# Performance work log

Measured on AMD Instinct MI355X. Metric: run time of the kernel, lower is better.

Reference implementation:

```python
import jax, jax.numpy as jnp
import numpy as np

N_SIN = 3  # fcn_n_sin

def _feats(x):
    # x: [B, Din] -> features [B, Din, 1 + 2*N_SIN]
    omega = (2.0 ** jnp.arange(N_SIN, dtype=x.dtype))  # [n_sin]
    ox = x[..., None] * omega  # [B, Din, n_sin]
    return jnp.concatenate([x[..., None], jnp.sin(ox), jnp.cos(ox)], axis=-1)

def setup_inputs() -> dict:
    key = jax.random.key(0)
    k1, k2, k3 = jax.random.split(key, 3)
    B, Din, Dout, H, F = 2048, 64, 64, 32, 1 + 2 * N_SIN
    x = jax.random.normal(k1, (B, Din), dtype=jnp.float32)
    # xavier-normal-ish init for W1/W2, zeros for biases (matches init_parameters)
    W1 = jax.random.normal(k2, (Din, Dout, H, F), dtype=jnp.float32) * np.sqrt(2.0 / (H + F))
    W2 = jax.random.normal(k3, (Din, Dout, 1, H), dtype=jnp.float32) * np.sqrt(2.0 / (1 + H))
    B1 = jnp.zeros((Din, Dout, H), dtype=jnp.float32)
    B2 = jnp.zeros((Din, Dout, 1), dtype=jnp.float32)
    return {"x": x, "W1": W1, "W2": W2, "B1": B1, "B2": B2}

def reference(x, W1, W2, B1, B2):
    f = _feats(x)  # [B, Din, F]
    # per-edge first layer: [B, Din, Dout, H]
    h = jnp.einsum('bif,iohf->bioh', f, W1) + B1[None]
    h = jax.nn.silu(h)
    # per-edge second layer -> scalar: [B, Din, Dout]
    phis = jnp.einsum('bioh,ioh->bio', h, W2[:, :, 0, :]) + B2[:, :, 0][None]
    return phis.sum(axis=1)  # [B, Dout]
```

## Files before the change

### kernel.cpp

```cpp
#include <hip/hip_runtime.h>
#include <math.h>

typedef _Float16 f16;
typedef f16   f16x4    __attribute__((ext_vector_type(4)));
typedef f16   f16x8    __attribute__((ext_vector_type(8)));
typedef float floatx2  __attribute__((ext_vector_type(2)));
typedef float floatx4  __attribute__((ext_vector_type(4)));
typedef float floatx16 __attribute__((ext_vector_type(16)));

#define LOG2E   1.44269504088896340736f
#define INV_2PI 0.15915494309189533577f

#define B_SZ  2048
#define DIN   64
#define DOUT  64
#define NH    32

#define NIG   4
#define IGW   (DIN / NIG)

#define W1IMG_ELEMS ((size_t)DIN * DOUT * 64 * 4)
#define FIMG_ELEMS  ((size_t)DIN * 64 * 64 * 4)
#define W2Q_ELEMS   ((size_t)DIN * DOUT * NH)

__device__ __forceinline__ floatx2 pk_add(floatx2 a, floatx2 b) {
    floatx2 d; asm("v_pk_add_f32 %0, %1, %2" : "=v"(d) : "v"(a), "v"(b)); return d;
}
__device__ __forceinline__ floatx2 pk_mul(floatx2 a, floatx2 b) {
    floatx2 d; asm("v_pk_mul_f32 %0, %1, %2" : "=v"(d) : "v"(a), "v"(b)); return d;
}
__device__ __forceinline__ floatx2 pk_fma(floatx2 a, floatx2 b, floatx2 c) {
    floatx2 d; asm("v_pk_fma_f32 %0, %1, %2, %3" : "=v"(d) : "v"(a), "v"(b), "v"(c)); return d;
}

__global__ __launch_bounds__(256) void prep_kernel(
        const float* __restrict__ W1, const float* __restrict__ B1,
        const float* __restrict__ W2, const float* __restrict__ B2,
        const float* __restrict__ x,
        f16* __restrict__ w1img, f16* __restrict__ fimg,
        float* __restrict__ w2q, float* __restrict__ b2sum,
        float* __restrict__ out) {
    const int bid = blockIdx.x, tid = threadIdx.x;
    if (bid < 512) {
        int u = bid * 256 + tid;
        int lane2 = u & 31, o = (u >> 5) & 63, i = u >> 11;
        int l0 = lane2 * 2;
        f16x8 v;
        if (lane2 < 16) {
#pragma unroll
            for (int t = 0; t < 2; ++t) {
                const float* w = W1 + (size_t)((i * 64 + o) * 32 + l0 + t) * 7;
#pragma unroll
                for (int j = 0; j < 4; ++j) v[t * 4 + j] = (f16)(w[j] * (-LOG2E));
            }
        } else {
#pragma unroll
            for (int t = 0; t < 2; ++t) {
                int m = l0 - 32 + t;
                const float* w = W1 + (size_t)((i * 64 + o) * 32 + m) * 7;
                v[t * 4 + 0] = (f16)(w[4] * (-LOG2E));
                v[t * 4 + 1] = (f16)(w[5] * (-LOG2E));
                v[t * 4 + 2] = (f16)(w[6] * (-LOG2E));
                v[t * 4 + 3] = (f16)(B1[(i * 64 + o) * 32 + m] * (-LOG2E));
            }
        }
        *(f16x8*)(w1img + (size_t)u * 8) = v;
    } else if (bid < 1024) {
        int u = (bid - 512) * 256 + tid;
        int lane2 = u & 31, btp = (u >> 5) & 63, i = u >> 11;
        int l0 = lane2 * 2;
        f16x8 v;
#pragma unroll
        for (int t = 0; t < 2; ++t) {
            int b = btp * 32 + ((l0 + t) & 31);
            float xv = x[b * 64 + i];
            float s1 = __builtin_amdgcn_sinf(xv * INV_2PI);
            float c1 = __builtin_amdgcn_cosf(xv * INV_2PI);
            float s2 = 2.0f * s1 * c1, c2 = 1.0f - 2.0f * s1 * s1;
            float s4 = 2.0f * s2 * c2, c4 = 1.0f - 2.0f * s2 * s2;
            if (lane2 < 16) { v[t*4+0] = (f16)xv; v[t*4+1] = (f16)s1;
                              v[t*4+2] = (f16)s2; v[t*4+3] = (f16)s4; }
            else            { v[t*4+0] = (f16)c1; v[t*4+1] = (f16)c2;
                              v[t*4+2] = (f16)c4; v[t*4+3] = (f16)1.0f; }
        }
        *(f16x8*)(fimg + (size_t)u * 8) = v;
    } else if (bid < 1152) {
        int t = (bid - 1024) * 256 + tid;
        floatx4 v = *(const floatx4*)(W2 + (size_t)t * 4);
        v *= (-1.0f / LOG2E);
        *(floatx4*)(w2q + (size_t)t * 4) = v;
    } else if (bid < 1280) {
        int t = (bid - 1152) * 256 + tid;
        floatx4 z = {};
        *(floatx4*)(out + (size_t)t * 4) = z;
    } else if (tid < 64) {
        float s = 0.0f;
        for (int i = 0; i < 64; ++i) s += B2[i * 64 + tid];
        b2sum[tid] = s;
    }
}

__device__ __forceinline__ void silu8(
        floatx2 A0, floatx2 A1, floatx2 A2, floatx2 A3,
        floatx2 W0, floatx2 W1, floatx2 W2, floatx2 W3,
        floatx2 one2, floatx2& phi) {
    floatx2 E0 = {__builtin_amdgcn_exp2f(A0[0]), __builtin_amdgcn_exp2f(A0[1])};
    floatx2 E1 = {__builtin_amdgcn_exp2f(A1[0]), __builtin_amdgcn_exp2f(A1[1])};
    floatx2 E2 = {__builtin_amdgcn_exp2f(A2[0]), __builtin_amdgcn_exp2f(A2[1])};
    floatx2 E3 = {__builtin_amdgcn_exp2f(A3[0]), __builtin_amdgcn_exp2f(A3[1])};
    floatx2 D0 = pk_add(E0, one2), D1 = pk_add(E1, one2);
    floatx2 D2 = pk_add(E2, one2), D3 = pk_add(E3, one2);
    floatx2 U0 = pk_mul(A0, W0), U1 = pk_mul(A1, W1);
    floatx2 U2 = pk_mul(A2, W2), U3 = pk_mul(A3, W3);
    floatx2 N01 = pk_fma(U0, D1, pk_mul(U1, D0));
    floatx2 N23 = pk_fma(U2, D3, pk_mul(U3, D2));
    floatx2 P01 = pk_mul(D0, D1), P23 = pk_mul(D2, D3);
    floatx2 N   = pk_fma(N01, P23, pk_mul(N23, P01));
    floatx2 DD  = pk_mul(P01, P23);
    floatx2 R = {__builtin_amdgcn_rcpf(DD[0]), __builtin_amdgcn_rcpf(DD[1])};
    phi = pk_fma(N, R, phi);
}

__global__ __launch_bounds__(128, 6) void main_kernel(
        const f16* __restrict__ w1img, const f16* __restrict__ fimg,
        const float* __restrict__ w2q, const float* __restrict__ b2sum,
        float* __restrict__ out) {
    const int tid  = threadIdx.x;
    const int lane = tid & 63;
    const int wv   = tid >> 6;
    const int btp  = blockIdx.x & 63;
    const int og   = (blockIdx.x >> 6) & 31;
    const int ig   = blockIdx.x >> 11;
    const int o    = __builtin_amdgcn_readfirstlane(og * 2 + wv);
    const int p    = lane >> 5;
    const size_t ibase = (size_t)ig * IGW;

    __shared__ float ws2[2][IGW + 1][32];
    {
        int idx = tid * 8;
        int wv_ = idx >> 9, ii_ = (idx >> 5) & 15, h_ = idx & 31;
        const float* src = w2q + (ibase + ii_) * 2048
                         + (size_t)(og * 2 + wv_) * 32 + h_;
        *(floatx4*)&ws2[wv_][ii_][h_]     = *(const floatx4*)src;
        *(floatx4*)&ws2[wv_][ii_][h_ + 4] = *(const floatx4*)(src + 4);
    }
    __syncthreads();

    const f16* ap = w1img + ibase * 16384 + ((size_t)o   * 64 + lane) * 4;
    const f16* bp = fimg  + ibase * 16384 + ((size_t)btp * 64 + lane) * 4;

    const floatx16 zeroC = {};
    const floatx2  one2  = {1.0f, 1.0f};
    floatx2 phiL = {}, phiH = {};

    f16x4 a0v = *(const f16x4*)ap;
    f16x4 b0v = *(const f16x4*)bp;
    f16x4 a_n = *(const f16x4*)(ap + 16384);
    f16x4 b_n = *(const f16x4*)(bp + 16384);
    floatx16 Ccur = __builtin_amdgcn_mfma_f32_32x32x8f16(a0v, b0v, zeroC, 0, 0, 0);

#pragma unroll 1
    for (int ii = 0; ii < IGW; ++ii) {
        floatx16 Cn = __builtin_amdgcn_mfma_f32_32x32x8f16(a_n, b_n, zeroC, 0, 0, 0);
        const size_t i2 = (size_t)(ii + 2);
        a_n = *(const f16x4*)(ap + i2 * 16384);
        b_n = *(const f16x4*)(bp + i2 * 16384);

        const float* wrow = &ws2[wv][ii][p * 4];
        const floatx4 W0 = *(const floatx4*)(wrow);
        const floatx4 W1v = *(const floatx4*)(wrow + 8);
        const floatx4 W2v = *(const floatx4*)(wrow + 16);
        const floatx4 W3v = *(const floatx4*)(wrow + 24);

        silu8((floatx2){Ccur[0],  Ccur[1]},  (floatx2){Ccur[4],  Ccur[5]},
              (floatx2){Ccur[8],  Ccur[9]},  (floatx2){Ccur[12], Ccur[13]},
              (floatx2){W0[0], W0[1]}, (floatx2){W1v[0], W1v[1]},
              (floatx2){W2v[0], W2v[1]}, (floatx2){W3v[0], W3v[1]},
              one2, phiL);
        silu8((floatx2){Ccur[2],  Ccur[3]},  (floatx2){Ccur[6],  Ccur[7]},
              (floatx2){Ccur[10], Ccur[11]}, (floatx2){Ccur[14], Ccur[15]},
              (floatx2){W0[2], W0[3]}, (floatx2){W1v[2], W1v[3]},
              (floatx2){W2v[2], W2v[3]}, (floatx2){W3v[2], W3v[3]},
              one2, phiH);

        Ccur = Cn;
    }

    float phi = (phiL[0] + phiL[1]) + (phiH[0] + phiH[1]);
    phi += __shfl_xor(phi, 32, 64);

    if (lane < 32) {
        float v = phi + 0.25f * b2sum[o];
        unsafeAtomicAdd(out + (size_t)(btp * 32 + lane) * 64 + o, v);
    }
}

extern "C" void kernel_launch(void* const* d_in, const int* in_sizes, int n_in,
                              void* d_out, int out_size, void* d_ws, size_t ws_size,
                              hipStream_t stream) {
    const float* x  = (const float*)d_in[0];
    const float* W1 = (const float*)d_in[1];
    const float* W2 = (const float*)d_in[2];
    const float* B1 = (const float*)d_in[3];
    const float* B2 = (const float*)d_in[4];
    float* out = (float*)d_out;

    f16*   w1img = (f16*)d_ws;
    f16*   fimg  = w1img + W1IMG_ELEMS;
    float* w2q   = (float*)(fimg + FIMG_ELEMS);
    float* b2sum = w2q + W2Q_ELEMS;

    prep_kernel<<<1281, 256, 0, stream>>>(W1, B1, W2, B2, x, w1img, fimg, w2q, b2sum, out);
    main_kernel<<<NIG * 32 * 64, 128, 0, stream>>>(w1img, fimg, w2q, b2sum, out);
}
```

Baseline: 114.1 us.

## Fold W2 scaling into epilogue and merge silu reciprocals across pairs

Drops the prep pass that pre-scaled W2 by -1/log2e and instead reads W2 directly, applying the scale once to the final per-lane sum. The silu8 combine now merges the two packed lanes into one numerator/denominator, so there is one reciprocal per 8 terms instead of two. The main loop is unrolled by two. Merging more denominators into one product raises the risk of float overflow or underflow in the combined denominator, and unrolling may increase register pressure.

```diff
diff --git a/kernel.cpp b/kernel.cpp
--- a/kernel.cpp
+++ b/kernel.cpp
@@ -21,7 +21,6 @@
 
 #define W1IMG_ELEMS ((size_t)DIN * DOUT * 64 * 4)
 #define FIMG_ELEMS  ((size_t)DIN * 64 * 64 * 4)
-#define W2Q_ELEMS   ((size_t)DIN * DOUT * NH)
 
 __device__ __forceinline__ floatx2 pk_add(floatx2 a, floatx2 b) {
     floatx2 d; asm("v_pk_add_f32 %0, %1, %2" : "=v"(d) : "v"(a), "v"(b)); return d;
@@ -35,11 +34,9 @@
 
 __global__ __launch_bounds__(256) void prep_kernel(
         const float* __restrict__ W1, const float* __restrict__ B1,
-        const float* __restrict__ W2, const float* __restrict__ B2,
-        const float* __restrict__ x,
+        const float* __restrict__ B2, const float* __restrict__ x,
         f16* __restrict__ w1img, f16* __restrict__ fimg,
-        float* __restrict__ w2q, float* __restrict__ b2sum,
-        float* __restrict__ out) {
+        float* __restrict__ b2sum, float* __restrict__ out) {
     const int bid = blockIdx.x, tid = threadIdx.x;
     if (bid < 512) {
         int u = bid * 256 + tid;
@@ -86,11 +83,6 @@
         *(f16x8*)(fimg + (size_t)u * 8) = v;
     } else if (bid < 1152) {
         int t = (bid - 1024) * 256 + tid;
-        floatx4 v = *(const floatx4*)(W2 + (size_t)t * 4);
-        v *= (-1.0f / LOG2E);
-        *(floatx4*)(w2q + (size_t)t * 4) = v;
-    } else if (bid < 1280) {
-        int t = (bid - 1152) * 256 + tid;
         floatx4 z = {};
         *(floatx4*)(out + (size_t)t * 4) = z;
     } else if (tid < 64) {
@@ -103,7 +95,7 @@
 __device__ __forceinline__ void silu8(
         floatx2 A0, floatx2 A1, floatx2 A2, floatx2 A3,
         floatx2 W0, floatx2 W1, floatx2 W2, floatx2 W3,
-        floatx2 one2, floatx2& phi) {
+        floatx2 one2, float& phi) {
     floatx2 E0 = {__builtin_amdgcn_exp2f(A0[0]), __builtin_amdgcn_exp2f(A0[1])};
     floatx2 E1 = {__builtin_amdgcn_exp2f(A1[0]), __builtin_amdgcn_exp2f(A1[1])};
     floatx2 E2 = {__builtin_amdgcn_exp2f(A2[0]), __builtin_amdgcn_exp2f(A2[1])};
@@ -117,13 +109,14 @@
     floatx2 P01 = pk_mul(D0, D1), P23 = pk_mul(D2, D3);
     floatx2 N   = pk_fma(N01, P23, pk_mul(N23, P01));
     floatx2 DD  = pk_mul(P01, P23);
-    floatx2 R = {__builtin_amdgcn_rcpf(DD[0]), __builtin_amdgcn_rcpf(DD[1])};
-    phi = pk_fma(N, R, phi);
+    float n8 = __builtin_fmaf(N[0], DD[1], N[1] * DD[0]);
+    float d8 = DD[0] * DD[1];
+    phi = __builtin_fmaf(n8, __builtin_amdgcn_rcpf(d8), phi);
 }
 
 __global__ __launch_bounds__(128, 6) void main_kernel(
         const f16* __restrict__ w1img, const f16* __restrict__ fimg,
-        const float* __restrict__ w2q, const float* __restrict__ b2sum,
+        const float* __restrict__ W2, const float* __restrict__ b2sum,
         float* __restrict__ out) {
     const int tid  = threadIdx.x;
     const int lane = tid & 63;
@@ -139,7 +132,7 @@
     {
         int idx = tid * 8;
         int wv_ = idx >> 9, ii_ = (idx >> 5) & 15, h_ = idx & 31;
-        const float* src = w2q + (ibase + ii_) * 2048
+        const float* src = W2 + (ibase + ii_) * 2048
                          + (size_t)(og * 2 + wv_) * 32 + h_;
         *(floatx4*)&ws2[wv_][ii_][h_]     = *(const floatx4*)src;
         *(floatx4*)&ws2[wv_][ii_][h_ + 4] = *(const floatx4*)(src + 4);
@@ -151,7 +144,7 @@
 
     const floatx16 zeroC = {};
     const floatx2  one2  = {1.0f, 1.0f};
-    floatx2 phiL = {}, phiH = {};
+    float phiL = 0.0f, phiH = 0.0f;
 
     f16x4 a0v = *(const f16x4*)ap;
     f16x4 b0v = *(const f16x4*)bp;
@@ -159,7 +152,7 @@
     f16x4 b_n = *(const f16x4*)(bp + 16384);
     floatx16 Ccur = __builtin_amdgcn_mfma_f32_32x32x8f16(a0v, b0v, zeroC, 0, 0, 0);
 
-#pragma unroll 1
+#pragma unroll 2
     for (int ii = 0; ii < IGW; ++ii) {
         floatx16 Cn = __builtin_amdgcn_mfma_f32_32x32x8f16(a_n, b_n, zeroC, 0, 0, 0);
         const size_t i2 = (size_t)(ii + 2);
@@ -186,11 +179,11 @@
         Ccur = Cn;
     }
 
-    float phi = (phiL[0] + phiL[1]) + (phiH[0] + phiH[1]);
+    float phi = phiL + phiH;
     phi += __shfl_xor(phi, 32, 64);
 
     if (lane < 32) {
-        float v = phi + 0.25f * b2sum[o];
+        float v = phi * (-1.0f / LOG2E) + (1.0f / NIG) * b2sum[o];
         unsafeAtomicAdd(out + (size_t)(btp * 32 + lane) * 64 + o, v);
     }
 }
@@ -207,9 +200,8 @@
 
     f16*   w1img = (f16*)d_ws;
     f16*   fimg  = w1img + W1IMG_ELEMS;
-    float* w2q   = (float*)(fimg + FIMG_ELEMS);
-    float* b2sum = w2q + W2Q_ELEMS;
-
-    prep_kernel<<<1281, 256, 0, stream>>>(W1, B1, W2, B2, x, w1img, fimg, w2q, b2sum, out);
-    main_kernel<<<NIG * 32 * 64, 128, 0, stream>>>(w1img, fimg, w2q, b2sum, out);
-}
+    float* b2sum = (float*)(fimg + FIMG_ELEMS);
+
+    prep_kernel<<<1153, 256, 0, stream>>>(W1, B1, B2, x, w1img, fimg, b2sum, out);
+    main_kernel<<<NIG * 32 * 64, 128, 0, stream>>>(w1img, fimg, W2, b2sum, out);
+}
```

Measured after the change: 111.8 us. 1.02x faster.
